# Optimization experiments

Measured on AMD Instinct MI355X. Metric: run time of the kernel, lower is better.

Reference implementation:

```python
import jax, jax.numpy as jnp
import numpy as np

SFREQ = 100
NPERSEG = 100  # min(n_times=200, 100)
NOVERLAP = NPERSEG // 2

# periodic hann window (scipy get_window('hann', N) with sym=False)
_WIN_NP = 0.5 - 0.5 * np.cos(2.0 * np.pi * np.arange(NPERSEG) / NPERSEG)
_WIN_SQ_SUM = float(np.sum(_WIN_NP ** 2))
_FREQS = np.fft.rfftfreq(NPERSEG, 1.0 / SFREQ)  # 0..50 Hz, 51 bins
_BANDS = [(0.5, 4.0), (4.0, 8.0), (8.0, 13.0), (13.0, 30.0)]  # delta/theta/alpha/beta
_BAND_IDX = [np.where((_FREQS >= lo) & (_FREQS <= hi))[0] for lo, hi in _BANDS]


def welch_band_features(x):
    """Batched Welch PSD band powers. x: (B,C,T) -> (B, C*4)."""
    B, C, T = x.shape
    step = NPERSEG - NOVERLAP
    n_seg = (T - NPERSEG) // step + 1
    seg_idx = np.arange(n_seg)[:, None] * step + np.arange(NPERSEG)  # (S, L)
    segs = x[..., seg_idx]                              # (B,C,S,L)
    segs = segs - segs.mean(-1, keepdims=True)          # detrend='constant'
    win = jnp.asarray(_WIN_NP, x.dtype)
    spec = jnp.fft.rfft(segs * win, axis=-1)            # (B,C,S,F)
    scale = 1.0 / (SFREQ * _WIN_SQ_SUM)
    psd = (spec.real ** 2 + spec.imag ** 2) * scale
    psd = psd.at[..., 1:-1].multiply(2.0)               # one-sided, nfft even
    psd = psd.mean(-2)                                  # average over segments -> (B,C,F)
    feats = jnp.stack([psd[..., idx].mean(-1) for idx in _BAND_IDX], axis=-1)  # (B,C,4)
    return feats.reshape(B, C * 4)


def setup_inputs() -> dict:
    key = jax.random.key(0)
    ks = jax.random.split(key, 16)
    B, C, T = 2048, 129, 200
    red = C // 8  # 16
    s = 0.05
    inp = {
        "x": jax.random.normal(ks[0], (B, C, T), jnp.float32),
        # channel attention fc (no bias)
        "w_att1": jax.random.normal(ks[1], (C, red), jnp.float32) * s,
        "w_att2": jax.random.normal(ks[2], (red, C), jnp.float32) * s,
        # stand-in EEGNeX backbone: time-mean pool + linear C->64
        "w_bb": jax.random.normal(ks[3], (C, 64), jnp.float32) * s,
        "b_bb": jnp.zeros((64,), jnp.float32),
        # freq encoder
        "w_fe1": jax.random.normal(ks[4], (C * 4, 128), jnp.float32) * s,
        "b_fe1": jnp.zeros((128,), jnp.float32),
        "w_fe2": jax.random.normal(ks[5], (128, 64), jnp.float32) * s,
        "b_fe2": jnp.zeros((64,), jnp.float32),
        # head
        "w_h1": jax.random.normal(ks[6], (128, 128), jnp.float32) * s,
        "b_h1": jnp.zeros((128,), jnp.float32),
        "w_h2": jax.random.normal(ks[7], (128, 64), jnp.float32) * s,
        "b_h2": jnp.zeros((64,), jnp.float32),
        "w_h3": jax.random.normal(ks[8], (64, 1), jnp.float32) * s,
        "b_h3": jnp.zeros((1,), jnp.float32),
    }
    return inp


def reference(x, w_att1, w_att2, w_bb, b_bb, w_fe1, b_fe1, w_fe2, b_fe2,
              w_h1, b_h1, w_h2, b_h2, w_h3, b_h3):
    # --- channel attention ---
    avg = x.mean(-1)                                    # (B,C)
    mx = x.max(-1)                                      # (B,C)
    fc = lambda v: jax.nn.relu(v @ w_att1) @ w_att2
    att = jax.nn.sigmoid(fc(avg) + fc(mx))[..., None]   # (B,C,1)
    x_att = x * att
    # --- backbone (stand-in for EEGNeXBase): time pool + linear ---
    time_feat = jax.nn.relu(x_att.mean(-1) @ w_bb + b_bb)  # (B,64)
    # --- frequency branch (computed from raw x, detached in original) ---
    freq = welch_band_features(jax.lax.stop_gradient(x))   # (B, C*4)
    freq = jax.nn.relu(freq @ w_fe1 + b_fe1)
    freq = jax.nn.relu(freq @ w_fe2 + b_fe2)               # (B,64)
    # --- head ---
    h = jnp.concatenate([time_feat, freq], axis=1)         # (B,128)
    h = jax.nn.relu(h @ w_h1 + b_h1)
    h = jax.nn.relu(h @ w_h2 + b_h2)
    return h @ w_h3 + b_h3                                  # (B,1)
```

## Files before the change

kernel.cpp:

```cpp
#include <hip/hip_runtime.h>
#include <math.h>

constexpr int BB = 2048;
constexpr int CC = 129;
constexpr int TT = 200;
constexpr int NPAIR = BB * CC;
constexpr int PPB = 64;

constexpr int OFF_AVG = 8192;
constexpr int OFF_MX  = OFF_AVG + NPAIR;
constexpr int OFF_FT  = OFF_MX + NPAIR;

typedef __bf16 bf16x8 __attribute__((ext_vector_type(8)));
typedef float  f32x4  __attribute__((ext_vector_type(4)));

union BFU { int4 v; bf16x8 b; };
union BSU { __bf16 b; unsigned short u; };

__global__ void kInit(unsigned short* __restrict__ bfr) {
    int tid = blockIdx.x * 256 + threadIdx.x;
    if (tid >= 16384) return;
    int i    = tid & 7;
    int lane = (tid >> 3) & 63;
    int h    = (tid >> 9) & 1;
    int nt   = (tid >> 10) & 3;
    int ks   = tid >> 12;
    int k = ks * 32 + (lane >> 4) * 8 + i;
    int n = nt * 16 + (lane & 15);
    float v = 0.f;
    if (k < 100) {
        if (n < 60) {
            int kb = (n >> 1) + 1;
            const float C = 0.06283185307179587f;
            float w = 0.5f - 0.5f * cosf(C * (float)k);
            int ph = (kb * k) % 100;
            float ang = C * (float)ph;
            v = w * ((n & 1) ? sinf(ang) : cosf(ang));
        } else if (n == 60) {
            v = 0.01f;
        }
    }
    __bf16 hb = (__bf16)v;
    BSU out;
    if (h == 0) out.b = hb;
    else        out.b = (__bf16)(v - (float)hb);
    bfr[tid] = out.u;
}

__global__ __launch_bounds__(256, 4) void kA(const float* __restrict__ x,
                                             const unsigned short* __restrict__ bfr,
                                             float* __restrict__ avg,
                                             float* __restrict__ mxg,
                                             float* __restrict__ feat) {
    __shared__ __align__(16) float rsall[4 * 384];

    const int tid  = threadIdx.x;
    const int blk  = blockIdx.x;
    const int wv   = tid >> 6;
    const int lane = tid & 63;
    const int P0   = blk * PPB + wv * 16;

    {
        int p = lane >> 2, q = lane & 3;
        const float* rowg = x + (size_t)(P0 + p) * TT;
        float m = -3.4e38f;
        #pragma unroll
        for (int j = 0; j < 13; j++) {
            int i4 = q + 4 * j;
            if (i4 < 50) {
                float4 v = *(const float4*)(rowg + i4 * 4);
                m = fmaxf(fmaxf(m, fmaxf(v.x, v.y)), fmaxf(v.z, v.w));
            }
        }
        m = fmaxf(m, __shfl_xor(m, 1, 64));
        m = fmaxf(m, __shfl_xor(m, 2, 64));
        if (q == 0) mxg[P0 + p] = m;
    }

    const int quad = lane >> 4, mrow = lane & 15;

    const float* abase[3];
    #pragma unroll
    for (int mi = 0; mi < 3; mi++) {
        int lr = mi * 16 + mrow;
        int pl = lr / 3;
        int sg = lr - pl * 3;
        abase[mi] = x + (size_t)(P0 + pl) * TT + sg * 50;
    }

    f32x4 acc[3][4];
    #pragma unroll
    for (int a = 0; a < 3; a++)
        #pragma unroll
        for (int b = 0; b < 4; b++) acc[a][b] = f32x4{0.f, 0.f, 0.f, 0.f};

    const int4* bg = (const int4*)bfr;
    #pragma unroll
    for (int ks = 0; ks < 4; ks++) {
        bf16x8 Bh[4], Bl[4];
        #pragma unroll
        for (int nt = 0; nt < 4; nt++) {
            BFU uh, ul;
            uh.v = bg[((ks * 4 + nt) * 2 + 0) * 64 + lane];
            ul.v = bg[((ks * 4 + nt) * 2 + 1) * 64 + lane];
            Bh[nt] = uh.b;
            Bl[nt] = ul.b;
        }
        #pragma unroll
        for (int mi = 0; mi < 3; mi++) {
            float f[8];
            if (ks < 3) {
                const float* s = abase[mi] + quad * 8 + ks * 32;
                float2 f0 = *(const float2*)(s);
                float2 f1 = *(const float2*)(s + 2);
                float2 f2 = *(const float2*)(s + 4);
                float2 f3 = *(const float2*)(s + 6);
                f[0] = f0.x; f[1] = f0.y; f[2] = f1.x; f[3] = f1.y;
                f[4] = f2.x; f[5] = f2.y; f[6] = f3.x; f[7] = f3.y;
            } else {
                const float* s = abase[mi] + 96;
                float2 f0 = *(const float2*)(s);
                float2 f1 = *(const float2*)(s + 2);
                bool v0 = (quad == 0);
                f[0] = v0 ? f0.x : 0.f; f[1] = v0 ? f0.y : 0.f;
                f[2] = v0 ? f1.x : 0.f; f[3] = v0 ? f1.y : 0.f;
                f[4] = 0.f; f[5] = 0.f; f[6] = 0.f; f[7] = 0.f;
            }
            bf16x8 Ah, Al;
            #pragma unroll
            for (int i = 0; i < 8; i++) {
                __bf16 hb = (__bf16)f[i];
                Ah[i] = hb;
                Al[i] = (__bf16)(f[i] - (float)hb);
            }
            __builtin_amdgcn_s_setprio(1);
            #pragma unroll
            for (int nt = 0; nt < 4; nt++) {
                acc[mi][nt] = __builtin_amdgcn_mfma_f32_16x16x32_bf16(Al, Bh[nt], acc[mi][nt], 0, 0, 0);
                acc[mi][nt] = __builtin_amdgcn_mfma_f32_16x16x32_bf16(Ah, Bl[nt], acc[mi][nt], 0, 0, 0);
                acc[mi][nt] = __builtin_amdgcn_mfma_f32_16x16x32_bf16(Ah, Bh[nt], acc[mi][nt], 0, 0, 0);
            }
            __builtin_amdgcn_s_setprio(0);
        }
    }

    float* rs = rsall + wv * 384;
    #pragma unroll
    for (int mi = 0; mi < 3; mi++) {
        #pragma unroll
        for (int i = 0; i < 4; i++) {
            float mu = __shfl(acc[mi][3][i], (lane & 48) | 12, 64);
            float v0 = acc[mi][0][i];
            if (mrow == 0) v0 += 25.f * mu;
            float w0 = v0 * v0;
            float w1 = acc[mi][1][i] * acc[mi][1][i];
            float w2 = acc[mi][2][i] * acc[mi][2][i];
            float w3 = acc[mi][3][i] * acc[mi][3][i];
            float s0 = (mrow <= 7) ? w0 : 0.f;
            float s1 = (mrow >= 6) ? w0 : 0.f;
            float s2 = ((mrow >= 14) ? w0 : 0.f) + ((mrow <= 9) ? w1 : 0.f);
            float s3 = ((mrow >= 8) ? w1 : 0.f) + w2 + ((mrow <= 11) ? w3 : 0.f);
            #pragma unroll
            for (int m = 1; m <= 8; m <<= 1) {
                s0 += __shfl_xor(s0, m, 16);
                s1 += __shfl_xor(s1, m, 16);
                s2 += __shfl_xor(s2, m, 16);
                s3 += __shfl_xor(s3, m, 16);
            }
            if (mrow == 0) {
                int lr = mi * 16 + quad * 4 + i;
                *(float4*)(rs + lr * 8) = float4{s0, s1, s2, s3};
                rs[lr * 8 + 4] = mu;
            }
        }
    }

    {
        int p2 = lane >> 2, q = lane & 3;
        int base = p2 * 24;
        float t = rs[base + q] + rs[base + 8 + q] + rs[base + 16 + q];
        float sc = (q == 0) ? (2.f / 45000.f)
                 : (q == 1) ? (2.f / 56250.f)
                 : (q == 2) ? (2.f / 67500.f)
                 :            (2.f / 202500.f);
        feat[(size_t)(P0 + p2) * 4 + q] = t * sc;
        if (q == 0) avg[P0 + p2] = (rs[base + 4] + rs[base + 20]) * 0.5f;
    }
}

__global__ __launch_bounds__(256, 8) void kB(const float* __restrict__ avg,
                                             const float* __restrict__ mxv,
                                             const float* __restrict__ feat,
                                             const float* __restrict__ w_att1,
                                             const float* __restrict__ w_att2,
                                             const float* __restrict__ w_bb,
                                             const float* __restrict__ b_bb,
                                             const float* __restrict__ w_fe1,
                                             const float* __restrict__ b_fe1,
                                             const float* __restrict__ w_fe2,
                                             const float* __restrict__ b_fe2,
                                             const float* __restrict__ w_h1,
                                             const float* __restrict__ b_h1,
                                             const float* __restrict__ w_h2,
                                             const float* __restrict__ b_h2,
                                             const float* __restrict__ w_h3,
                                             const float* __restrict__ b_h3,
                                             float* __restrict__ out) {
    __shared__ float s_avg[132], s_mx[132], s_fq[520];
    __shared__ float s_t1a[16], s_t1b[16], s_t1[16];
    __shared__ float s_v[132];
    __shared__ float s_tf[2][64];
    __shared__ float s_p1[2][128];
    __shared__ float s_f1[128];
    __shared__ float s_p2[4][64];
    __shared__ float s_h[128];
    __shared__ float s_pg1[2][128];
    __shared__ float s_g1[128];
    __shared__ float s_pg2[4][64];

    const int b = blockIdx.x;
    const int tid = threadIdx.x;

    for (int i = tid; i < 129; i += 256) { s_avg[i] = avg[b * 129 + i]; s_mx[i] = mxv[b * 129 + i]; }
    for (int i = tid; i < 516; i += 256) s_fq[i] = feat[(size_t)b * 516 + i];
    __syncthreads();

    if (tid < 32) {
        int h = tid & 15;
        const float* src = (tid >= 16) ? s_mx : s_avg;
        float acc = 0.f;
        #pragma unroll 4
        for (int c = 0; c < 129; c++) acc += src[c] * w_att1[c * 16 + h];
        ((tid >= 16) ? s_t1b : s_t1a)[h] = fmaxf(acc, 0.f);
    }
    __syncthreads();
    if (tid < 16) s_t1[tid] = s_t1a[tid] + s_t1b[tid];
    __syncthreads();

    if (tid < 129) {
        float l = 0.f;
        #pragma unroll
        for (int j = 0; j < 16; j++) l += s_t1[j] * w_att2[j * 129 + tid];
        s_v[tid] = s_avg[tid] / (1.f + expf(-l));
    }
    __syncthreads();

    if (tid < 128) {
        int o = tid & 63, ks = tid >> 6;
        int i0 = ks ? 65 : 0, i1 = ks ? 129 : 65;
        float acc = 0.f;
        #pragma unroll 4
        for (int i = i0; i < i1; i++) acc += s_v[i] * w_bb[i * 64 + o];
        s_tf[ks][o] = acc;
    }
    {
        int o = tid & 127, ks = tid >> 7;
        float acc = 0.f;
        #pragma unroll 4
        for (int i = ks * 258; i < ks * 258 + 258; i++) acc += s_fq[i] * w_fe1[i * 128 + o];
        s_p1[ks][o] = acc;
    }
    __syncthreads();
    if (tid < 64) s_h[tid] = fmaxf(s_tf[0][tid] + s_tf[1][tid] + b_bb[tid], 0.f);
    if (tid >= 128) { int o = tid - 128; s_f1[o] = fmaxf(s_p1[0][o] + s_p1[1][o] + b_fe1[o], 0.f); }
    __syncthreads();

    {
        int o = tid & 63, ks = tid >> 6;
        float acc = 0.f;
        #pragma unroll 4
        for (int i = ks * 32; i < ks * 32 + 32; i++) acc += s_f1[i] * w_fe2[i * 64 + o];
        s_p2[ks][o] = acc;
    }
    __syncthreads();
    if (tid < 64) s_h[64 + tid] = fmaxf(s_p2[0][tid] + s_p2[1][tid] + s_p2[2][tid] + s_p2[3][tid] + b_fe2[tid], 0.f);
    __syncthreads();

    {
        int o = tid & 127, ks = tid >> 7;
        float acc = 0.f;
        #pragma unroll 4
        for (int i = ks * 64; i < ks * 64 + 64; i++) acc += s_h[i] * w_h1[i * 128 + o];
        s_pg1[ks][o] = acc;
    }
    __syncthreads();
    if (tid < 128) s_g1[tid] = fmaxf(s_pg1[0][tid] + s_pg1[1][tid] + b_h1[tid], 0.f);
    __syncthreads();

    {
        int o = tid & 63, ks = tid >> 6;
        float acc = 0.f;
        #pragma unroll 4
        for (int i = ks * 32; i < ks * 32 + 32; i++) acc += s_g1[i] * w_h2[i * 64 + o];
        s_pg2[ks][o] = acc;
    }
    __syncthreads();

    if (tid < 64) {
        float g2 = fmaxf(s_pg2[0][tid] + s_pg2[1][tid] + s_pg2[2][tid] + s_pg2[3][tid] + b_h2[tid], 0.f);
        float pz = g2 * w_h3[tid];
        for (int off = 32; off >= 1; off >>= 1) pz += __shfl_xor(pz, off, 64);
        if (tid == 0) out[b] = pz + b_h3[0];
    }
}

extern "C" void kernel_launch(void* const* d_in, const int* in_sizes, int n_in,
                              void* d_out, int out_size, void* d_ws, size_t ws_size,
                              hipStream_t stream) {
    const float* x      = (const float*)d_in[0];
    const float* w_att1 = (const float*)d_in[1];
    const float* w_att2 = (const float*)d_in[2];
    const float* w_bb   = (const float*)d_in[3];
    const float* b_bb   = (const float*)d_in[4];
    const float* w_fe1  = (const float*)d_in[5];
    const float* b_fe1  = (const float*)d_in[6];
    const float* w_fe2  = (const float*)d_in[7];
    const float* b_fe2  = (const float*)d_in[8];
    const float* w_h1   = (const float*)d_in[9];
    const float* b_h1   = (const float*)d_in[10];
    const float* w_h2   = (const float*)d_in[11];
    const float* b_h2   = (const float*)d_in[12];
    const float* w_h3   = (const float*)d_in[13];
    const float* b_h3   = (const float*)d_in[14];

    float* ws = (float*)d_ws;
    unsigned short* bfr = (unsigned short*)ws;
    float* avg = ws + OFF_AVG;
    float* mxv = ws + OFF_MX;
    float* feat = ws + OFF_FT;

    kInit<<<64, 256, 0, stream>>>(bfr);
    kA<<<NPAIR / PPB, 256, 0, stream>>>(x, bfr, avg, mxv, feat);
    kB<<<BB, 256, 0, stream>>>(avg, mxv, feat,
                               w_att1, w_att2, w_bb, b_bb,
                               w_fe1, b_fe1, w_fe2, b_fe2,
                               w_h1, b_h1, w_h2, b_h2, w_h3, b_h3,
                               (float*)d_out);
}
```

Before: 457.7 us.

## Restructure Welch kernel to one segment tile per wave with register-held inputs

Each wave now handles a single 16-row tile of one segment index instead of three interleaved tiles, loading its row slice into registers once and reusing it for both the max reduction and the MFMA A operands. This removes the separate full-row max pass and the LDS cross-segment reduction; per-segment partial features, means and maxima are written to separate workspace arrays and combined in the head kernel. Block indices are also remapped across 8 groups. The trade is three times more blocks, more global writes and reads for the partials, and extra work in kB.

```diff
diff --git a/kernel.cpp b/kernel.cpp
--- a/kernel.cpp
+++ b/kernel.cpp
@@ -5,11 +5,15 @@
 constexpr int CC = 129;
 constexpr int TT = 200;
 constexpr int NPAIR = BB * CC;
-constexpr int PPB = 64;
-
-constexpr int OFF_AVG = 8192;
-constexpr int OFF_MX  = OFF_AVG + NPAIR;
-constexpr int OFF_FT  = OFF_MX + NPAIR;
+constexpr int NPG   = NPAIR / 16;
+constexpr int NTILE = NPG * 3;
+constexpr int NBLK  = NTILE / 4;
+
+constexpr int OFF_AVG0 = 8192;
+constexpr int OFF_AVG2 = OFF_AVG0 + NPAIR;
+constexpr int OFF_MX0  = OFF_AVG2 + NPAIR;
+constexpr int OFF_MX2  = OFF_MX0 + NPAIR;
+constexpr int OFF_F3   = OFF_MX2 + NPAIR;
 
 typedef __bf16 bf16x8 __attribute__((ext_vector_type(8)));
 typedef float  f32x4  __attribute__((ext_vector_type(4)));
@@ -49,50 +53,66 @@
 
 __global__ __launch_bounds__(256, 4) void kA(const float* __restrict__ x,
                                              const unsigned short* __restrict__ bfr,
-                                             float* __restrict__ avg,
-                                             float* __restrict__ mxg,
-                                             float* __restrict__ feat) {
-    __shared__ __align__(16) float rsall[4 * 384];
-
+                                             float* __restrict__ avg0,
+                                             float* __restrict__ avg2,
+                                             float* __restrict__ mx0,
+                                             float* __restrict__ mx2,
+                                             float* __restrict__ feat3) {
     const int tid  = threadIdx.x;
-    const int blk  = blockIdx.x;
+    const int blk  = (blockIdx.x & 7) * (NBLK / 8) + (blockIdx.x >> 3);
     const int wv   = tid >> 6;
     const int lane = tid & 63;
-    const int P0   = blk * PPB + wv * 16;
-
-    {
-        int p = lane >> 2, q = lane & 3;
-        const float* rowg = x + (size_t)(P0 + p) * TT;
+    const int tile = blk * 4 + wv;
+    const int pg   = tile / 3;
+    const int sg   = tile - pg * 3;
+    const int quad = lane >> 4, mrow = lane & 15;
+
+    const float* rp = x + (size_t)(pg * 16 + mrow) * TT + sg * 50;
+
+    float2 ar[14];
+    #pragma unroll
+    for (int c = 0; c < 12; c++) {
+        int ks = c >> 2, j = c & 3;
+        ar[c] = *(const float2*)(rp + ks * 32 + quad * 8 + j * 2);
+    }
+    ar[12] = *(const float2*)(rp + 96);
+    ar[13] = *(const float2*)(rp + 98);
+
+    bf16x8 Ah[4], Al[4];
+    #pragma unroll
+    for (int ks = 0; ks < 4; ks++) {
+        float f[8];
+        if (ks < 3) {
+            f[0] = ar[ks * 4 + 0].x; f[1] = ar[ks * 4 + 0].y;
+            f[2] = ar[ks * 4 + 1].x; f[3] = ar[ks * 4 + 1].y;
+            f[4] = ar[ks * 4 + 2].x; f[5] = ar[ks * 4 + 2].y;
+            f[6] = ar[ks * 4 + 3].x; f[7] = ar[ks * 4 + 3].y;
+        } else {
+            bool v0 = (quad == 0);
+            f[0] = v0 ? ar[12].x : 0.f; f[1] = v0 ? ar[12].y : 0.f;
+            f[2] = v0 ? ar[13].x : 0.f; f[3] = v0 ? ar[13].y : 0.f;
+            f[4] = 0.f; f[5] = 0.f; f[6] = 0.f; f[7] = 0.f;
+        }
+        #pragma unroll
+        for (int i = 0; i < 8; i++) {
+            __bf16 hb = (__bf16)f[i];
+            Ah[ks][i] = hb;
+            Al[ks][i] = (__bf16)(f[i] - (float)hb);
+        }
+    }
+
+    if (sg != 1) {
         float m = -3.4e38f;
         #pragma unroll
-        for (int j = 0; j < 13; j++) {
-            int i4 = q + 4 * j;
-            if (i4 < 50) {
-                float4 v = *(const float4*)(rowg + i4 * 4);
-                m = fmaxf(fmaxf(m, fmaxf(v.x, v.y)), fmaxf(v.z, v.w));
-            }
-        }
-        m = fmaxf(m, __shfl_xor(m, 1, 64));
-        m = fmaxf(m, __shfl_xor(m, 2, 64));
-        if (q == 0) mxg[P0 + p] = m;
-    }
-
-    const int quad = lane >> 4, mrow = lane & 15;
-
-    const float* abase[3];
-    #pragma unroll
-    for (int mi = 0; mi < 3; mi++) {
-        int lr = mi * 16 + mrow;
-        int pl = lr / 3;
-        int sg = lr - pl * 3;
-        abase[mi] = x + (size_t)(P0 + pl) * TT + sg * 50;
-    }
-
-    f32x4 acc[3][4];
-    #pragma unroll
-    for (int a = 0; a < 3; a++)
-        #pragma unroll
-        for (int b = 0; b < 4; b++) acc[a][b] = f32x4{0.f, 0.f, 0.f, 0.f};
+        for (int c = 0; c < 14; c++) m = fmaxf(m, fmaxf(ar[c].x, ar[c].y));
+        m = fmaxf(m, __shfl_xor(m, 16, 64));
+        m = fmaxf(m, __shfl_xor(m, 32, 64));
+        if (quad == 0) (sg == 0 ? mx0 : mx2)[pg * 16 + mrow] = m;
+    }
+
+    f32x4 acc[4];
+    #pragma unroll
+    for (int b = 0; b < 4; b++) acc[b] = f32x4{0.f, 0.f, 0.f, 0.f};
 
     const int4* bg = (const int4*)bfr;
     #pragma unroll
@@ -106,91 +126,56 @@
             Bh[nt] = uh.b;
             Bl[nt] = ul.b;
         }
-        #pragma unroll
-        for (int mi = 0; mi < 3; mi++) {
-            float f[8];
-            if (ks < 3) {
-                const float* s = abase[mi] + quad * 8 + ks * 32;
-                float2 f0 = *(const float2*)(s);
-                float2 f1 = *(const float2*)(s + 2);
-                float2 f2 = *(const float2*)(s + 4);
-                float2 f3 = *(const float2*)(s + 6);
-                f[0] = f0.x; f[1] = f0.y; f[2] = f1.x; f[3] = f1.y;
-                f[4] = f2.x; f[5] = f2.y; f[6] = f3.x; f[7] = f3.y;
-            } else {
-                const float* s = abase[mi] + 96;
-                float2 f0 = *(const float2*)(s);
-                float2 f1 = *(const float2*)(s + 2);
-                bool v0 = (quad == 0);
-                f[0] = v0 ? f0.x : 0.f; f[1] = v0 ? f0.y : 0.f;
-                f[2] = v0 ? f1.x : 0.f; f[3] = v0 ? f1.y : 0.f;
-                f[4] = 0.f; f[5] = 0.f; f[6] = 0.f; f[7] = 0.f;
-            }
-            bf16x8 Ah, Al;
-            #pragma unroll
-            for (int i = 0; i < 8; i++) {
-                __bf16 hb = (__bf16)f[i];
-                Ah[i] = hb;
-                Al[i] = (__bf16)(f[i] - (float)hb);
-            }
-            __builtin_amdgcn_s_setprio(1);
-            #pragma unroll
-            for (int nt = 0; nt < 4; nt++) {
-                acc[mi][nt] = __builtin_amdgcn_mfma_f32_16x16x32_bf16(Al, Bh[nt], acc[mi][nt], 0, 0, 0);
-                acc[mi][nt] = __builtin_amdgcn_mfma_f32_16x16x32_bf16(Ah, Bl[nt], acc[mi][nt], 0, 0, 0);
-                acc[mi][nt] = __builtin_amdgcn_mfma_f32_16x16x32_bf16(Ah, Bh[nt], acc[mi][nt], 0, 0, 0);
-            }
-            __builtin_amdgcn_s_setprio(0);
-        }
-    }
-
-    float* rs = rsall + wv * 384;
-    #pragma unroll
-    for (int mi = 0; mi < 3; mi++) {
-        #pragma unroll
-        for (int i = 0; i < 4; i++) {
-            float mu = __shfl(acc[mi][3][i], (lane & 48) | 12, 64);
-            float v0 = acc[mi][0][i];
-            if (mrow == 0) v0 += 25.f * mu;
-            float w0 = v0 * v0;
-            float w1 = acc[mi][1][i] * acc[mi][1][i];
-            float w2 = acc[mi][2][i] * acc[mi][2][i];
-            float w3 = acc[mi][3][i] * acc[mi][3][i];
-            float s0 = (mrow <= 7) ? w0 : 0.f;
-            float s1 = (mrow >= 6) ? w0 : 0.f;
-            float s2 = ((mrow >= 14) ? w0 : 0.f) + ((mrow <= 9) ? w1 : 0.f);
-            float s3 = ((mrow >= 8) ? w1 : 0.f) + w2 + ((mrow <= 11) ? w3 : 0.f);
-            #pragma unroll
-            for (int m = 1; m <= 8; m <<= 1) {
-                s0 += __shfl_xor(s0, m, 16);
-                s1 += __shfl_xor(s1, m, 16);
-                s2 += __shfl_xor(s2, m, 16);
-                s3 += __shfl_xor(s3, m, 16);
-            }
-            if (mrow == 0) {
-                int lr = mi * 16 + quad * 4 + i;
-                *(float4*)(rs + lr * 8) = float4{s0, s1, s2, s3};
-                rs[lr * 8 + 4] = mu;
-            }
-        }
-    }
-
-    {
-        int p2 = lane >> 2, q = lane & 3;
-        int base = p2 * 24;
-        float t = rs[base + q] + rs[base + 8 + q] + rs[base + 16 + q];
-        float sc = (q == 0) ? (2.f / 45000.f)
-                 : (q == 1) ? (2.f / 56250.f)
-                 : (q == 2) ? (2.f / 67500.f)
-                 :            (2.f / 202500.f);
-        feat[(size_t)(P0 + p2) * 4 + q] = t * sc;
-        if (q == 0) avg[P0 + p2] = (rs[base + 4] + rs[base + 20]) * 0.5f;
+        __builtin_amdgcn_s_setprio(1);
+        #pragma unroll
+        for (int nt = 0; nt < 4; nt++) {
+            acc[nt] = __builtin_amdgcn_mfma_f32_16x16x32_bf16(Al[ks], Bh[nt], acc[nt], 0, 0, 0);
+            acc[nt] = __builtin_amdgcn_mfma_f32_16x16x32_bf16(Ah[ks], Bl[nt], acc[nt], 0, 0, 0);
+            acc[nt] = __builtin_amdgcn_mfma_f32_16x16x32_bf16(Ah[ks], Bh[nt], acc[nt], 0, 0, 0);
+        }
+        __builtin_amdgcn_s_setprio(0);
+    }
+
+    float* fout = feat3 + (size_t)sg * NPAIR * 4;
+    #pragma unroll
+    for (int i = 0; i < 4; i++) {
+        float mu = __shfl(acc[3][i], (lane & 48) | 12, 64);
+        float v0 = acc[0][i];
+        if (mrow == 0) v0 += 25.f * mu;
+        float w0 = v0 * v0;
+        float w1 = acc[1][i] * acc[1][i];
+        float w2 = acc[2][i] * acc[2][i];
+        float w3 = acc[3][i] * acc[3][i];
+        float s0 = (mrow <= 7) ? w0 : 0.f;
+        float s1 = (mrow >= 6) ? w0 : 0.f;
+        float s2 = ((mrow >= 14) ? w0 : 0.f) + ((mrow <= 9) ? w1 : 0.f);
+        float s3 = ((mrow >= 8) ? w1 : 0.f) + w2 + ((mrow <= 11) ? w3 : 0.f);
+        #pragma unroll
+        for (int m = 1; m <= 8; m <<= 1) {
+            s0 += __shfl_xor(s0, m, 16);
+            s1 += __shfl_xor(s1, m, 16);
+            s2 += __shfl_xor(s2, m, 16);
+            s3 += __shfl_xor(s3, m, 16);
+        }
+        if (mrow == 0) {
+            int pr = pg * 16 + quad * 4 + i;
+            float4 fo;
+            fo.x = s0 * (2.f / 45000.f);
+            fo.y = s1 * (2.f / 56250.f);
+            fo.z = s2 * (2.f / 67500.f);
+            fo.w = s3 * (2.f / 202500.f);
+            *(float4*)(fout + (size_t)pr * 4) = fo;
+            if (sg == 0) avg0[pr] = mu;
+            if (sg == 2) avg2[pr] = mu;
+        }
     }
 }
 
-__global__ __launch_bounds__(256, 8) void kB(const float* __restrict__ avg,
-                                             const float* __restrict__ mxv,
-                                             const float* __restrict__ feat,
+__global__ __launch_bounds__(256, 8) void kB(const float* __restrict__ avg0,
+                                             const float* __restrict__ avg2,
+                                             const float* __restrict__ mx0,
+                                             const float* __restrict__ mx2,
+                                             const float* __restrict__ feat3,
                                              const float* __restrict__ w_att1,
                                              const float* __restrict__ w_att2,
                                              const float* __restrict__ w_bb,
@@ -221,8 +206,16 @@
     const int b = blockIdx.x;
     const int tid = threadIdx.x;
 
-    for (int i = tid; i < 129; i += 256) { s_avg[i] = avg[b * 129 + i]; s_mx[i] = mxv[b * 129 + i]; }
-    for (int i = tid; i < 516; i += 256) s_fq[i] = feat[(size_t)b * 516 + i];
+    for (int i = tid; i < 129; i += 256) {
+        s_avg[i] = (avg0[b * 129 + i] + avg2[b * 129 + i]) * 0.5f;
+        s_mx[i]  = fmaxf(mx0[b * 129 + i], mx2[b * 129 + i]);
+    }
+    {
+        const float* f0 = feat3 + (size_t)b * 516;
+        const float* f1 = f0 + (size_t)NPAIR * 4;
+        const float* f2 = f1 + (size_t)NPAIR * 4;
+        for (int i = tid; i < 516; i += 256) s_fq[i] = f0[i] + f1[i] + f2[i];
+    }
     __syncthreads();
 
     if (tid < 32) {
@@ -325,13 +318,15 @@
 
     float* ws = (float*)d_ws;
     unsigned short* bfr = (unsigned short*)ws;
-    float* avg = ws + OFF_AVG;
-    float* mxv = ws + OFF_MX;
-    float* feat = ws + OFF_FT;
+    float* avg0  = ws + OFF_AVG0;
+    float* avg2  = ws + OFF_AVG2;
+    float* mx0   = ws + OFF_MX0;
+    float* mx2   = ws + OFF_MX2;
+    float* feat3 = ws + OFF_F3;
 
     kInit<<<64, 256, 0, stream>>>(bfr);
-    kA<<<NPAIR / PPB, 256, 0, stream>>>(x, bfr, avg, mxv, feat);
-    kB<<<BB, 256, 0, stream>>>(avg, mxv, feat,
+    kA<<<NBLK, 256, 0, stream>>>(x, bfr, avg0, avg2, mx0, mx2, feat3);
+    kB<<<BB, 256, 0, stream>>>(avg0, avg2, mx0, mx2, feat3,
                                w_att1, w_att2, w_bb, b_bb,
                                w_fe1, b_fe1, w_fe2, b_fe2,
                                w_h1, b_h1, w_h2, b_h2, w_h3, b_h3,
```

New measurement: 462.6 us. Within noise of the previous version (+1.1%).
